# Performance work log

Hardware: AMD Instinct MI355X
Metric: run time of the kernel (lower is better)

Reference implementation:

```python
import jax, jax.numpy as jnp
import numpy as np

NUM_NODE = 5000
EMBED_DIM = 256
NUM_CLS = 20
EDGE_ROWS = (NUM_NODE - 1) * (NUM_NODE - 1) + 1  # 24990002
BZ, SEQ, NBR = 64, 512, 16


def setup_inputs() -> dict:
    key = jax.random.key(0)
    k = jax.random.split(key, 8)
    X = jax.random.randint(k[0], (BZ, SEQ), 0, NUM_NODE)
    NX = jax.random.randint(k[1], (BZ, SEQ, NBR), 0, NUM_NODE)
    EW = jax.random.randint(k[2], (BZ, SEQ, NBR), 0, EDGE_ROWS)
    # parameters (xavier-ish scale); padding_idx=0 rows zeroed
    node_emb = jax.random.normal(k[3], (NUM_NODE, EMBED_DIM), jnp.float32) * 0.02
    node_emb = node_emb.at[0].set(0.0)
    edge_w = jax.random.normal(k[4], (EDGE_ROWS, 1), jnp.float32) * 0.02
    edge_w = edge_w.at[0].set(0.0)
    node_w = jax.random.normal(k[5], (NUM_NODE, 1), jnp.float32) * 0.02
    node_w = node_w.at[0].set(0.0)
    fc_W = jax.random.normal(k[6], (NUM_CLS, EMBED_DIM), jnp.float32) * 0.05
    fc_b = jnp.zeros((NUM_CLS,), jnp.float32)
    return {"X": X, "NX": NX, "EW": EW, "node_emb": node_emb,
            "edge_w": edge_w, "node_w": node_w, "fc_W": fc_W, "fc_b": fc_b}


def reference(X, NX, EW, node_emb, edge_w, node_w, fc_W, fc_b):
    Ra = node_emb[NX]                      # (bz, seq, nbr, d) neighbor embeddings
    Ean = edge_w[EW]                       # (bz, seq, nbr, 1) edge weights
    Mn = jnp.max(Ra * Ean, axis=2)         # (bz, seq, d) max over neighbors
    Rn = node_emb[X]                       # (bz, seq, d)
    Nn = node_w[X]                         # (bz, seq, 1)
    y = (1.0 - Nn) * Mn + Nn * Rn          # weighted combine
    y = jnp.sum(y, axis=1)                 # (bz, d) sum-pool over sequence
    y = y @ fc_W.T + fc_b                  # (bz, num_cls)
    y = jax.nn.relu(y)
    # Dropout is identity at inference; LogSoftmax over dim=1
    return jax.nn.log_softmax(y, axis=1)
```

## Files before the change

### kernel.cpp

```cpp
#include <hip/hip_runtime.h>
#include <math.h>

#define NUM_NODE 5000
#define BZ   64
#define SEQ  512
#define NBR  16
#define DIM  256
#define NCLS 20

#define ROWB8   DIM
#define ESCALE  256.0f
#define CW      8
#define NCHUNK  (SEQ / CW)
#define CVT_N4  (NUM_NODE * DIM / 4)
#define NCHUNK16 (SEQ / 16)

typedef float v2f __attribute__((ext_vector_type(2)));

__device__ __forceinline__ int bcast_i(int v, int lane) {
    return __builtin_amdgcn_readlane(v, lane);
}
__device__ __forceinline__ float bcast_f(float v, int lane) {
    return __int_as_float(__builtin_amdgcn_readlane(__float_as_int(v), lane));
}

__global__ __launch_bounds__(256) void zero_ws_kernel(float* __restrict__ ws, int n) {
    int i = blockIdx.x * blockDim.x + threadIdx.x;
    if (i < n) ws[i] = 0.0f;
}

__global__ __launch_bounds__(256) void cvt_emb_kernel(
    const float4* __restrict__ src, unsigned* __restrict__ dst, int n4) {
    int i = blockIdx.x * blockDim.x + threadIdx.x;
    if (i < n4) {
        float4 v = src[i];
        int r = 0;
        r = __builtin_amdgcn_cvt_pk_fp8_f32(v.x * ESCALE, v.y * ESCALE, r, false);
        r = __builtin_amdgcn_cvt_pk_fp8_f32(v.z * ESCALE, v.w * ESCALE, r, true);
        dst[i] = (unsigned)r;
    }
}

__global__ __launch_bounds__(512, 8) void gnn_gather_kernel(
    const int*   __restrict__ X,
    const int*   __restrict__ NX,
    const int*   __restrict__ EW,
    const char*  __restrict__ emb8,
    const float* __restrict__ edge_w,
    const float* __restrict__ node_w,
    float*       __restrict__ part)
{
    __shared__ float lds[CW][DIM];

    const int b     = blockIdx.x / NCHUNK;
    const int chunk = blockIdx.x % NCHUNK;
    const int wave  = threadIdx.x >> 6;
    const int lane  = threadIdx.x & 63;
    const int half  = lane >> 5;
    const int sub   = lane & 31;
    const int voff  = sub * 8;

    const int s  = chunk * CW + wave;
    const int bs = b * SEQ + s;

    int   ewi = 0, nxv = 0;
    float ewv = 0.f;
    if (lane < NBR) {
        ewi = __builtin_nontemporal_load(&EW[bs * NBR + lane]);
        nxv = __builtin_nontemporal_load(&NX[bs * NBR + lane]);
    }
    if (lane < NBR)
        ewv = __builtin_nontemporal_load(&edge_w[ewi]);

    const int   x  = X[bs];
    const float nn = node_w[x];

    uint2 e[8];
    #pragma unroll
    for (int j = 0; j < 8; ++j) {
        const int n0 = bcast_i(nxv, 2 * j);
        const int n1 = bcast_i(nxv, 2 * j + 1);
        const int n  = half ? n1 : n0;
        e[j] = *(const uint2*)(emb8 + (size_t)n * ROWB8 + voff);
    }
    const uint2 es = *(const uint2*)(emb8 + (size_t)x * ROWB8 + voff);

    float m[8];
    #pragma unroll
    for (int i = 0; i < 8; ++i) m[i] = -INFINITY;

    #pragma unroll
    for (int j = 0; j < 8; ++j) {
        const float w0 = bcast_f(ewv, 2 * j);
        const float w1 = bcast_f(ewv, 2 * j + 1);
        const float w  = half ? w1 : w0;
        const v2f a0 = __builtin_amdgcn_cvt_pk_f32_fp8((int)e[j].x, false);
        const v2f a1 = __builtin_amdgcn_cvt_pk_f32_fp8((int)e[j].x, true);
        const v2f a2 = __builtin_amdgcn_cvt_pk_f32_fp8((int)e[j].y, false);
        const v2f a3 = __builtin_amdgcn_cvt_pk_f32_fp8((int)e[j].y, true);
        m[0] = fmaxf(m[0], a0.x * w);
        m[1] = fmaxf(m[1], a0.y * w);
        m[2] = fmaxf(m[2], a1.x * w);
        m[3] = fmaxf(m[3], a1.y * w);
        m[4] = fmaxf(m[4], a2.x * w);
        m[5] = fmaxf(m[5], a2.y * w);
        m[6] = fmaxf(m[6], a3.x * w);
        m[7] = fmaxf(m[7], a3.y * w);
    }

    #pragma unroll
    for (int i = 0; i < 8; ++i)
        m[i] = fmaxf(m[i], __shfl_xor(m[i], 32));

    const v2f s0 = __builtin_amdgcn_cvt_pk_f32_fp8((int)es.x, false);
    const v2f s1 = __builtin_amdgcn_cvt_pk_f32_fp8((int)es.x, true);
    const v2f s2 = __builtin_amdgcn_cvt_pk_f32_fp8((int)es.y, false);
    const v2f s3 = __builtin_amdgcn_cvt_pk_f32_fp8((int)es.y, true);

    const float om = 1.0f - nn;
    float acc[8];
    acc[0] = om * m[0] + nn * s0.x;
    acc[1] = om * m[1] + nn * s0.y;
    acc[2] = om * m[2] + nn * s1.x;
    acc[3] = om * m[3] + nn * s1.y;
    acc[4] = om * m[4] + nn * s2.x;
    acc[5] = om * m[5] + nn * s2.y;
    acc[6] = om * m[6] + nn * s3.x;
    acc[7] = om * m[7] + nn * s3.y;

    if (half == 0) {
        *(float4*)&lds[wave][8 * sub]     = make_float4(acc[0], acc[1], acc[2], acc[3]);
        *(float4*)&lds[wave][8 * sub + 4] = make_float4(acc[4], acc[5], acc[6], acc[7]);
    }
    __syncthreads();

    if (threadIdx.x < DIM) {
        float ssum = 0.f;
        #pragma unroll
        for (int w2 = 0; w2 < CW; ++w2) ssum += lds[w2][threadIdx.x];
        part[((size_t)b * NCHUNK + chunk) * DIM + threadIdx.x] = ssum * (1.0f / ESCALE);
    }
}

__global__ __launch_bounds__(256) void gnn_gather_f32_kernel(
    const int*   __restrict__ X,
    const int*   __restrict__ NX,
    const int*   __restrict__ EW,
    const float* __restrict__ node_emb,
    const float* __restrict__ edge_w,
    const float* __restrict__ node_w,
    float*       __restrict__ dst)
{
    __shared__ float lds[4][DIM];
    const int b     = blockIdx.x / NCHUNK16;
    const int chunk = blockIdx.x % NCHUNK16;
    const int wave  = threadIdx.x >> 6;
    const int lane  = threadIdx.x & 63;
    const int s0  = chunk * 16 + wave * 4;
    const int bs0 = b * SEQ + s0;

    const int   nx  = NX[bs0 * NBR + lane];
    const float ew  = edge_w[EW[bs0 * NBR + lane]];
    int xv = 0; float nwv = 0.f;
    if (lane < 4) { xv = X[bs0 + lane]; nwv = node_w[xv]; }

    float4 acc = make_float4(0.f, 0.f, 0.f, 0.f);
    for (int p = 0; p < 4; ++p) {
        float4 m = make_float4(-INFINITY, -INFINITY, -INFINITY, -INFINITY);
        for (int k = 0; k < NBR; ++k) {
            const int   n = bcast_i(nx, p * 16 + k);
            const float w = bcast_f(ew, p * 16 + k);
            const float4 e = *(const float4*)(node_emb + (size_t)n * DIM + 4 * lane);
            m.x = fmaxf(m.x, e.x * w); m.y = fmaxf(m.y, e.y * w);
            m.z = fmaxf(m.z, e.z * w); m.w = fmaxf(m.w, e.w * w);
        }
        const int   x  = bcast_i(xv, p);
        const float nn = bcast_f(nwv, p);
        const float om = 1.0f - nn;
        const float4 r = *(const float4*)(node_emb + (size_t)x * DIM + 4 * lane);
        acc.x += om * m.x + nn * r.x; acc.y += om * m.y + nn * r.y;
        acc.z += om * m.z + nn * r.z; acc.w += om * m.w + nn * r.w;
    }
    *(float4*)&lds[wave][4 * lane] = acc;
    __syncthreads();
    const int t = threadIdx.x;
    atomicAdd(&dst[b * DIM + t], lds[0][t] + lds[1][t] + lds[2][t] + lds[3][t]);
}

__global__ __launch_bounds__(256) void gnn_head_kernel(
    const float* __restrict__ part,
    const int                 nchunk,
    const float* __restrict__ fc_W,
    const float* __restrict__ fc_b,
    float*       __restrict__ out)
{
    __shared__ float4 lds4[4][64];
    __shared__ float vals[NCLS];
    __shared__ float lse;

    const int b = blockIdx.x;
    const int t = threadIdx.x;
    const int wave = t >> 6;
    const int lane = t & 63;

    float4 y = make_float4(0.f, 0.f, 0.f, 0.f);
    for (int c = wave; c < nchunk; c += 4) {
        const float4 v = *(const float4*)(part + ((size_t)b * nchunk + c) * DIM + 4 * lane);
        y.x += v.x; y.y += v.y; y.z += v.z; y.w += v.w;
    }
    lds4[wave][lane] = y;
    __syncthreads();
    const float4 a0 = lds4[0][lane], a1 = lds4[1][lane];
    const float4 a2 = lds4[2][lane], a3 = lds4[3][lane];
    const float4 y4 = make_float4(a0.x + a1.x + a2.x + a3.x,
                                  a0.y + a1.y + a2.y + a3.y,
                                  a0.z + a1.z + a2.z + a3.z,
                                  a0.w + a1.w + a2.w + a3.w);

    #pragma unroll
    for (int ci = 0; ci < 5; ++ci) {
        const int c = wave * 5 + ci;
        const float4 w4 = *(const float4*)(fc_W + c * DIM + 4 * lane);
        float d = y4.x * w4.x + y4.y * w4.y + y4.z * w4.z + y4.w * w4.w;
        #pragma unroll
        for (int off = 32; off; off >>= 1) d += __shfl_xor(d, off);
        if (lane == 0) vals[c] = fmaxf(d + fc_b[c], 0.0f);
    }
    __syncthreads();

    if (t == 0) {
        float mx = -INFINITY;
        for (int c = 0; c < NCLS; ++c) mx = fmaxf(mx, vals[c]);
        float s = 0.0f;
        for (int c = 0; c < NCLS; ++c) s += expf(vals[c] - mx);
        lse = mx + logf(s);
    }
    __syncthreads();

    if (t < NCLS) out[b * NCLS + t] = vals[t] - lse;
}

extern "C" void kernel_launch(void* const* d_in, const int* in_sizes, int n_in,
                              void* d_out, int out_size, void* d_ws, size_t ws_size,
                              hipStream_t stream) {
    const int*   X        = (const int*)  d_in[0];
    const int*   NX       = (const int*)  d_in[1];
    const int*   EW       = (const int*)  d_in[2];
    const float* node_emb = (const float*)d_in[3];
    const float* edge_w   = (const float*)d_in[4];
    const float* node_w   = (const float*)d_in[5];
    const float* fc_W     = (const float*)d_in[6];
    const float* fc_b     = (const float*)d_in[7];
    float* out = (float*)d_out;

    const size_t part_bytes = (size_t)BZ * NCHUNK * DIM * sizeof(float);
    const size_t emb_bytes  = (size_t)NUM_NODE * DIM;
    float* part = (float*)d_ws;
    char*  emb8 = (char*)d_ws + part_bytes;

    if (ws_size >= part_bytes + emb_bytes) {
        cvt_emb_kernel<<<(CVT_N4 + 255) / 256, 256, 0, stream>>>(
            (const float4*)node_emb, (unsigned*)emb8, CVT_N4);
        gnn_gather_kernel<<<BZ * NCHUNK, 512, 0, stream>>>(
            X, NX, EW, emb8, edge_w, node_w, part);
        gnn_head_kernel<<<BZ, 256, 0, stream>>>(part, NCHUNK, fc_W, fc_b, out);
    } else {
        zero_ws_kernel<<<(BZ * DIM + 255) / 256, 256, 0, stream>>>(part, BZ * DIM);
        gnn_gather_f32_kernel<<<BZ * NCHUNK16, 256, 0, stream>>>(
            X, NX, EW, node_emb, edge_w, node_w, part);
        gnn_head_kernel<<<BZ, 256, 0, stream>>>(part, 1, fc_W, fc_b, out);
    }
}
```

Before: 176.1 us.

## Gather fp8 embeddings with 16-byte loads across four neighbor groups per wave

Changes the per-wave lane mapping so each lane loads 16 fp8 bytes (uint4) of a neighbor row, with four neighbor groups of 16 lanes instead of two halves of 32, cutting the number of load instructions per lane from 8 to 4. The NX and EW index loads are merged into a single lane-split load, and neighbor indices and weights are broadcast with shuffles. The cost is more registers per lane (16 accumulators), an extra cross-lane max-reduction step, and more shuffle traffic.

Result: slower. 179.8 us (+2.1%).

```diff
diff --git a/kernel.cpp b/kernel.cpp
--- a/kernel.cpp
+++ b/kernel.cpp
@@ -56,81 +56,76 @@
     const int chunk = blockIdx.x % NCHUNK;
     const int wave  = threadIdx.x >> 6;
     const int lane  = threadIdx.x & 63;
-    const int half  = lane >> 5;
-    const int sub   = lane & 31;
-    const int voff  = sub * 8;
+    const int q     = lane >> 4;
+    const int r     = lane & 15;
+    const int voff  = r * 16;
 
     const int s  = chunk * CW + wave;
     const int bs = b * SEQ + s;
 
-    int   ewi = 0, nxv = 0;
+    int iv = 0;
+    if (lane < 32) {
+        const int* p = (lane < 16) ? &NX[bs * NBR + r] : &EW[bs * NBR + r];
+        iv = __builtin_nontemporal_load(p);
+    }
     float ewv = 0.f;
-    if (lane < NBR) {
-        ewi = __builtin_nontemporal_load(&EW[bs * NBR + lane]);
-        nxv = __builtin_nontemporal_load(&NX[bs * NBR + lane]);
-    }
-    if (lane < NBR)
-        ewv = __builtin_nontemporal_load(&edge_w[ewi]);
+    if (lane >= 16 && lane < 32) ewv = edge_w[iv];
 
     const int   x  = X[bs];
     const float nn = node_w[x];
 
-    uint2 e[8];
-    #pragma unroll
-    for (int j = 0; j < 8; ++j) {
-        const int n0 = bcast_i(nxv, 2 * j);
-        const int n1 = bcast_i(nxv, 2 * j + 1);
-        const int n  = half ? n1 : n0;
-        e[j] = *(const uint2*)(emb8 + (size_t)n * ROWB8 + voff);
-    }
-    const uint2 es = *(const uint2*)(emb8 + (size_t)x * ROWB8 + voff);
-
-    float m[8];
-    #pragma unroll
-    for (int i = 0; i < 8; ++i) m[i] = -INFINITY;
-
-    #pragma unroll
-    for (int j = 0; j < 8; ++j) {
-        const float w0 = bcast_f(ewv, 2 * j);
-        const float w1 = bcast_f(ewv, 2 * j + 1);
-        const float w  = half ? w1 : w0;
-        const v2f a0 = __builtin_amdgcn_cvt_pk_f32_fp8((int)e[j].x, false);
-        const v2f a1 = __builtin_amdgcn_cvt_pk_f32_fp8((int)e[j].x, true);
-        const v2f a2 = __builtin_amdgcn_cvt_pk_f32_fp8((int)e[j].y, false);
-        const v2f a3 = __builtin_amdgcn_cvt_pk_f32_fp8((int)e[j].y, true);
-        m[0] = fmaxf(m[0], a0.x * w);
-        m[1] = fmaxf(m[1], a0.y * w);
-        m[2] = fmaxf(m[2], a1.x * w);
-        m[3] = fmaxf(m[3], a1.y * w);
-        m[4] = fmaxf(m[4], a2.x * w);
-        m[5] = fmaxf(m[5], a2.y * w);
-        m[6] = fmaxf(m[6], a3.x * w);
-        m[7] = fmaxf(m[7], a3.y * w);
-    }
-
-    #pragma unroll
-    for (int i = 0; i < 8; ++i)
-        m[i] = fmaxf(m[i], __shfl_xor(m[i], 32));
-
-    const v2f s0 = __builtin_amdgcn_cvt_pk_f32_fp8((int)es.x, false);
-    const v2f s1 = __builtin_amdgcn_cvt_pk_f32_fp8((int)es.x, true);
-    const v2f s2 = __builtin_amdgcn_cvt_pk_f32_fp8((int)es.y, false);
-    const v2f s3 = __builtin_amdgcn_cvt_pk_f32_fp8((int)es.y, true);
+    int na[4];
+    #pragma unroll
+    for (int g = 0; g < 4; ++g) na[g] = __shfl(iv, 4 * g + q);
+
+    uint4 e[4];
+    #pragma unroll
+    for (int g = 0; g < 4; ++g)
+        e[g] = *(const uint4*)(emb8 + (size_t)na[g] * ROWB8 + voff);
+    const uint4 es = *(const uint4*)(emb8 + (size_t)x * ROWB8 + voff);
+
+    float m[16];
+    #pragma unroll
+    for (int k = 0; k < 16; ++k) m[k] = -INFINITY;
+
+    #pragma unroll
+    for (int g = 0; g < 4; ++g) {
+        const float w = __shfl(ewv, 16 + 4 * g + q);
+        const unsigned wd[4] = {e[g].x, e[g].y, e[g].z, e[g].w};
+        #pragma unroll
+        for (int d = 0; d < 4; ++d) {
+            const v2f lo = __builtin_amdgcn_cvt_pk_f32_fp8((int)wd[d], false);
+            const v2f hi = __builtin_amdgcn_cvt_pk_f32_fp8((int)wd[d], true);
+            m[4 * d + 0] = fmaxf(m[4 * d + 0], lo.x * w);
+            m[4 * d + 1] = fmaxf(m[4 * d + 1], lo.y * w);
+            m[4 * d + 2] = fmaxf(m[4 * d + 2], hi.x * w);
+            m[4 * d + 3] = fmaxf(m[4 * d + 3], hi.y * w);
+        }
+    }
+    #pragma unroll
+    for (int k = 0; k < 16; ++k) m[k] = fmaxf(m[k], __shfl_xor(m[k], 16));
+    #pragma unroll
+    for (int k = 0; k < 16; ++k) m[k] = fmaxf(m[k], __shfl_xor(m[k], 32));
 
     const float om = 1.0f - nn;
-    float acc[8];
-    acc[0] = om * m[0] + nn * s0.x;
-    acc[1] = om * m[1] + nn * s0.y;
-    acc[2] = om * m[2] + nn * s1.x;
-    acc[3] = om * m[3] + nn * s1.y;
-    acc[4] = om * m[4] + nn * s2.x;
-    acc[5] = om * m[5] + nn * s2.y;
-    acc[6] = om * m[6] + nn * s3.x;
-    acc[7] = om * m[7] + nn * s3.y;
-
-    if (half == 0) {
-        *(float4*)&lds[wave][8 * sub]     = make_float4(acc[0], acc[1], acc[2], acc[3]);
-        *(float4*)&lds[wave][8 * sub + 4] = make_float4(acc[4], acc[5], acc[6], acc[7]);
+    {
+        const unsigned wd[4] = {es.x, es.y, es.z, es.w};
+        #pragma unroll
+        for (int d = 0; d < 4; ++d) {
+            const v2f lo = __builtin_amdgcn_cvt_pk_f32_fp8((int)wd[d], false);
+            const v2f hi = __builtin_amdgcn_cvt_pk_f32_fp8((int)wd[d], true);
+            m[4 * d + 0] = om * m[4 * d + 0] + nn * lo.x;
+            m[4 * d + 1] = om * m[4 * d + 1] + nn * lo.y;
+            m[4 * d + 2] = om * m[4 * d + 2] + nn * hi.x;
+            m[4 * d + 3] = om * m[4 * d + 3] + nn * hi.y;
+        }
+    }
+
+    if (q == 0) {
+        #pragma unroll
+        for (int d = 0; d < 4; ++d)
+            *(float4*)&lds[wave][16 * r + 4 * d] =
+                make_float4(m[4 * d], m[4 * d + 1], m[4 * d + 2], m[4 * d + 3]);
     }
     __syncthreads();
 
```
